# Kernel optimization log

Measured on AMD Instinct MI355X. Metric: run time of the kernel, lower is better.

The kernel has to match this reference:

```python
import jax, jax.numpy as jnp
import numpy as np

N = 20000          # nodes
E = 320000         # edges
IN_C = 512         # input features
HID = 512          # 2*out_channels (first GCN layer width)
OUT = 256          # out_channels == num_hidden
PROJ = 256         # num_proj_hidden


def _gcn_conv(x, W, b, src, dst):
    """PyG GCNConv: x' = D^{-1/2}(A+I)D^{-1/2} X W + b (self-loops added)."""
    n = x.shape[0]
    x = x @ W  # [N, F_out]
    ones = jnp.ones((src.shape[0],), x.dtype)
    deg = jax.ops.segment_sum(ones, dst, num_segments=n) + 1.0  # +1 self-loop
    dis = jax.lax.rsqrt(deg)
    coef = dis[src] * dis[dst]                      # [E]
    agg = jax.ops.segment_sum(x[src] * coef[:, None], dst, num_segments=n)
    agg = agg + x * (dis * dis)[:, None]            # self-loop messages
    return agg + b


def setup_inputs() -> dict:
    key = jax.random.key(0)
    ks = jax.random.split(key, 12)
    s = 0.02
    return {
        "node_features": jax.random.normal(ks[0], (N, IN_C), jnp.float32),
        "edge_index": jax.random.randint(ks[1], (2, E), 0, N, jnp.int64),
        "W1": jax.random.normal(ks[2], (IN_C, HID), jnp.float32) * s,
        "b1": jnp.zeros((HID,), jnp.float32),
        "W2": jax.random.normal(ks[3], (HID, OUT), jnp.float32) * s,
        "b2": jnp.zeros((OUT,), jnp.float32),
        "a": jnp.asarray(0.25, jnp.float32),  # shared PReLU weight
        "W3": jax.random.normal(ks[4], (OUT, PROJ), jnp.float32) * s,
        "b3": jnp.zeros((PROJ,), jnp.float32),
        "W4": jax.random.normal(ks[5], (PROJ, OUT), jnp.float32) * s,
        "b4": jnp.zeros((OUT,), jnp.float32),
    }


def reference(node_features, edge_index, W1, b1, W2, b2, a, W3, b3, W4, b4):
    src, dst = edge_index[0], edge_index[1]
    prelu = lambda x: jnp.where(x > 0, x, a * x)
    h = prelu(_gcn_conv(node_features, W1, b1, src, dst))
    h = prelu(_gcn_conv(h, W2, b2, src, dst))
    # projection MLP: Linear -> ELU -> Linear
    h2 = jax.nn.elu(h @ W3 + b3)
    return h2 @ W4 + b4
```

## Files before the change

kernel.cpp:

```cpp
#include <hip/hip_runtime.h>
#include <stdint.h>

typedef unsigned short u16;
typedef unsigned int   u32;
typedef __attribute__((ext_vector_type(8))) short short8;
typedef __attribute__((ext_vector_type(4))) float f32x4;

__device__ __forceinline__ float bf2f(u16 h){
    return __uint_as_float(((u32)h) << 16);
}
__device__ __forceinline__ u16 f2bf(float f){
    u32 u = __float_as_uint(f);
    u += 0x7fffu + ((u >> 16) & 1u);
    return (u16)(u >> 16);
}

__device__ __forceinline__ void gl_lds16(const void* g, void* l){
    __builtin_amdgcn_global_load_lds(
        (__attribute__((address_space(1))) void*)(uintptr_t)g,
        (__attribute__((address_space(3))) void*)(uintptr_t)l,
        16, 0, 0);
}

__global__ void probe_all(const u16* __restrict__ w1, const int* __restrict__ ei,
                          const void* b1, const void* b2, const void* b3,
                          const void* b4, const void* av,
                          int* __restrict__ efmt, int* __restrict__ cnt, int N,
                          u16* d1, u16* d2, u16* d3, u16* d4, u16* da){
    __shared__ int sf32, sfmt;
    int t = threadIdx.x;
    if (t == 0){ sf32 = 0; sfmt = 0; }
    __syncthreads();
    for (int i = t; i < N; i += 256) cnt[i] = 0;
    {
        int huge = 0;
        #pragma unroll
        for (int k = 0; k < 16; k++){
            u16 h = w1[t * 16 + k];
            if (((h >> 7) & 0xFF) >= 0x7F) huge = 1;
        }
        if (huge) atomicOr(&sf32, 1);
    }
    if (ei[2*t + 1] != 0) atomicOr(&sfmt, 1);
    __syncthreads();
    int f32 = sf32;
    if (t == 0) efmt[0] = sfmt;
    #define CV(s,i) (f32 ? f2bf(((const float*)(s))[i]) : ((const u16*)(s))[i])
    d1[t]       = CV(b1, t);
    d1[t + 256] = CV(b1, t + 256);
    d2[t] = CV(b2, t);
    d3[t] = CV(b3, t);
    d4[t] = CV(b4, t);
    if (t == 0) da[0] = CV(av, 0);
    #undef CV
}

__device__ __forceinline__ int eload(const int* ei, int fmt, int idx){
    return fmt ? ei[idx] : ei[2*idx];
}

__global__ void deg_count(const int* __restrict__ ei, const int* __restrict__ efmt,
                          int* __restrict__ cnt, int E, int N){
    int e = blockIdx.x * 256 + threadIdx.x;
    if (e < E){
        int d = eload(ei, efmt[0], E + e);
        if ((unsigned)d < (unsigned)N) atomicAdd(&cnt[d], 1);
    }
}

__global__ void scan1(const int* __restrict__ cnt, int* __restrict__ incl,
                      int* __restrict__ bsum, int N){
    __shared__ int s[256];
    int t = threadIdx.x, i = blockIdx.x * 256 + t;
    int v = (i < N) ? cnt[i] : 0;
    s[t] = v;
    __syncthreads();
    #pragma unroll
    for (int off = 1; off < 256; off <<= 1){
        int u = (t >= off) ? s[t - off] : 0;
        __syncthreads();
        s[t] += u;
        __syncthreads();
    }
    if (i < N) incl[i] = s[t];
    if (t == 255) bsum[blockIdx.x] = s[255];
}

__global__ void scan23(const int* __restrict__ cnt, const int* __restrict__ incl,
                       const int* __restrict__ bsum, int nb,
                       int* __restrict__ rowstart, int* __restrict__ cursor,
                       float* __restrict__ dis, int N){
    __shared__ int s[128];
    int t = threadIdx.x;
    if (t < 128) s[t] = (t < nb) ? bsum[t] : 0;
    __syncthreads();
    #pragma unroll
    for (int off = 1; off < 128; off <<= 1){
        int u = 0;
        if (t < 128 && t >= off) u = s[t - off];
        __syncthreads();
        if (t < 128) s[t] += u;
        __syncthreads();
    }
    int boffb = s[blockIdx.x] - bsum[blockIdx.x];
    int i = blockIdx.x * 256 + t;
    if (i < N){
        int v = cnt[i];
        int rsv = boffb + incl[i] - v;
        rowstart[i] = rsv;
        cursor[i]   = rsv;
        dis[i] = rsqrtf((float)v + 1.0f);
    }
    if (blockIdx.x == 0 && t == 0) rowstart[N] = s[nb - 1];
}

__global__ void csr_fill(const int* __restrict__ ei, const int* __restrict__ efmt,
                         int* __restrict__ cursor, int* __restrict__ csr_src,
                         int E, int N){
    int e = blockIdx.x * 256 + threadIdx.x;
    if (e < E){
        int fmt = efmt[0];
        int d = eload(ei, fmt, E + e);
        if ((unsigned)d < (unsigned)N){
            int p = atomicAdd(&cursor[d], 1);
            csr_src[p] = eload(ei, fmt, e);
        }
    }
}

__global__ void transpose_x(const void* w1, const void* w2, const void* w3,
                            const void* w4, const void* X,
                            u16* o1, u16* o2, u16* o3, u16* o4,
                            u16* xbf, int NN){
    __shared__ int sf;
    __shared__ u16 tb[32][33];
    int lt = threadIdx.y * 32 + threadIdx.x;
    if (lt == 0) sf = 0;
    __syncthreads();
    {
        int huge = 0;
        const u16* w = (const u16*)w1;
        #pragma unroll
        for (int k = 0; k < 8; k++){
            u16 h = w[lt * 8 + k];
            if (((h >> 7) & 0xFF) >= 0x7F) huge = 1;
        }
        if (huge) atomicOr(&sf, 1);
    }
    __syncthreads();
    int f32 = sf;

    if (blockIdx.z == 4){
        size_t nb8 = (size_t)NN * 64;
        size_t step = 256u * 256u;
        for (size_t i = (size_t)(blockIdx.y * 16 + blockIdx.x) * 256 + lt; i < nb8; i += step){
            short8 o;
            if (f32){
                const float* p = (const float*)X + i * 8;
                f32x4 a0 = *(const f32x4*)p;
                f32x4 a1 = *(const f32x4*)(p + 4);
                #pragma unroll
                for (int j = 0; j < 4; j++){
                    o[j]     = (short)f2bf(a0[j]);
                    o[4 + j] = (short)f2bf(a1[j]);
                }
            } else {
                o = *(const short8*)((const u16*)X + i * 8);
            }
            *(short8*)(xbf + i * 8) = o;
        }
        return;
    }

    const void* in; u16* out; int K, N;
    switch (blockIdx.z){
        case 0:  in = w1; out = o1; K = 512; N = 512; break;
        case 1:  in = w2; out = o2; K = 512; N = 256; break;
        case 2:  in = w3; out = o3; K = 256; N = 256; break;
        default: in = w4; out = o4; K = 256; N = 256; break;
    }
    int bx = blockIdx.x * 32;
    int by = blockIdx.y * 32;
    if (bx >= N || by >= K) return;
    int x = threadIdx.x, y = threadIdx.y;
    #pragma unroll
    for (int i = 0; i < 32; i += 8){
        size_t idx = (size_t)(by + y + i) * N + bx + x;
        tb[y + i][x] = f32 ? f2bf(((const float*)in)[idx]) : ((const u16*)in)[idx];
    }
    __syncthreads();
    #pragma unroll
    for (int i = 0; i < 32; i += 8)
        out[(size_t)(bx + y + i) * K + by + x] = tb[x][y + i];
}

#define GTM 128
#define GTN 128
#define GBK 64

template<int MODE, int OUTF>
__global__ __launch_bounds__(256) void gemm128(
    const u16* __restrict__ A, const u16* __restrict__ BT,
    const u16* __restrict__ bias, void* __restrict__ Cv,
    int M, int K, int N, int nN)
{
    __shared__ __align__(16) u16 As[GTM * GBK];
    __shared__ __align__(16) u16 Bs[GTN * GBK];
    int nwg = gridDim.x;
    int flat = blockIdx.x;
    int q8 = nwg >> 3, r8 = nwg & 7;
    int xcd = flat & 7, idx8 = flat >> 3;
    int wg = (xcd < r8 ? xcd * (q8 + 1) : r8 * (q8 + 1) + (xcd - r8) * q8) + idx8;
    int bm = (wg / nN) * GTM;
    int bn = (wg % nN) * GTN;

    int tid  = threadIdx.x;
    int lane = tid & 63;
    int wm   = (tid >> 7) & 1;
    int wn   = (tid >> 6) & 1;

    f32x4 acc[4][4] = {};

    int srow = tid >> 3;
    int scol = (tid & 7) * 8;
    const u16* aP = A  + (size_t)(bm + srow) * K + scol;
    const u16* bP = BT + (size_t)(bn + srow) * K + scol;
    u16* lA = &As[tid * 8];
    u16* lB = &Bs[tid * 8];

    int q   = lane >> 4;
    int r16 = lane & 15;
    const u16* ra = &As[(wm*64 + r16) * GBK + q*8];
    const u16* rb = &Bs[(wn*64 + r16) * GBK + q*8];

    for (int k0 = 0; k0 < K; k0 += GBK){
        #pragma unroll
        for (int r = 0; r < 4; r++){
            gl_lds16(aP + (size_t)r*32*K + k0, lA + r*32*GBK);
            gl_lds16(bP + (size_t)r*32*K + k0, lB + r*32*GBK);
        }
        __syncthreads();
        #pragma unroll
        for (int kk = 0; kk < 2; kk++){
            short8 af[4], bf[4];
            #pragma unroll
            for (int i = 0; i < 4; i++) af[i] = *(const short8*)(ra + i*16*GBK + kk*32);
            #pragma unroll
            for (int j = 0; j < 4; j++) bf[j] = *(const short8*)(rb + j*16*GBK + kk*32);
            #pragma unroll
            for (int i = 0; i < 4; i++)
                #pragma unroll
                for (int j = 0; j < 4; j++)
                    acc[i][j] = __builtin_amdgcn_mfma_f32_16x16x32_bf16(af[i], bf[j], acc[i][j], 0, 0, 0);
        }
        __syncthreads();
    }

    int q4 = q * 4;
    #pragma unroll
    for (int i = 0; i < 4; i++){
        #pragma unroll
        for (int j = 0; j < 4; j++){
            int gcol = bn + wn*64 + j*16 + r16;
            float bvv = (MODE >= 1) ? bf2f(bias[gcol]) : 0.f;
            #pragma unroll
            for (int r = 0; r < 4; r++){
                int grow = bm + wm*64 + i*16 + q4 + r;
                if (grow < M){
                    float v = acc[i][j][r] + bvv;
                    if (MODE == 2) v = (v > 0.f) ? v : expm1f(v);
                    if (OUTF) ((float*)Cv)[(size_t)grow * N + gcol] = v;
                    else      ((u16*)Cv)[(size_t)grow * N + gcol] = f2bf(v);
                }
            }
        }
    }
}

template<int F, int CH>
__global__ __launch_bounds__(256) void aggregate_ch(
    const u16* __restrict__ XW, const int* __restrict__ rowstart,
    const int* __restrict__ csr_src, const float* __restrict__ dis,
    const u16* __restrict__ bias, const u16* __restrict__ aptr,
    u16* __restrict__ out, int N)
{
    constexpr int NCH = F / CH;
    constexpr int LPN = CH / 8;
    constexpr int NPB = 256 / LPN;
    int bid = blockIdx.x;
    int chunk = bid % NCH;
    int node = (bid / NCH) * NPB + (threadIdx.x >> 3);
    if (node >= N) return;
    int tf = chunk * CH + (threadIdx.x & (LPN - 1)) * 8;
    float a  = bf2f(aptr[0]);
    float di = dis[node];
    int e0 = rowstart[node], e1 = rowstart[node + 1];
    float acc[8] = {0,0,0,0,0,0,0,0};
    int ng = (e1 - e0) >> 3;
    int si[8]; float ci[8];
    if (ng > 0){
        #pragma unroll
        for (int u = 0; u < 8; u++) si[u] = csr_src[e0 + u];
        #pragma unroll
        for (int u = 0; u < 8; u++) ci[u] = dis[si[u]];
    }
    for (int g = 0; g < ng; g++){
        short8 vi[8];
        #pragma unroll
        for (int u = 0; u < 8; u++)
            vi[u] = *(const short8*)(XW + (size_t)si[u] * F + tf);
        int sn[8]; float cn[8];
        bool more = (g + 1) < ng;
        if (more){
            int base = e0 + (g + 1) * 8;
            #pragma unroll
            for (int u = 0; u < 8; u++) sn[u] = csr_src[base + u];
            #pragma unroll
            for (int u = 0; u < 8; u++) cn[u] = dis[sn[u]];
        }
        #pragma unroll
        for (int u = 0; u < 8; u++)
            #pragma unroll
            for (int j = 0; j < 8; j++)
                acc[j] += ci[u] * bf2f((u16)vi[u][j]);
        if (more){
            #pragma unroll
            for (int u = 0; u < 8; u++){ si[u] = sn[u]; ci[u] = cn[u]; }
        }
    }
    int e = e0 + ng * 8;
    for (; e + 4 <= e1; e += 4){
        int s0 = csr_src[e], s1 = csr_src[e+1], s2 = csr_src[e+2], s3 = csr_src[e+3];
        float c0 = dis[s0], c1 = dis[s1], c2 = dis[s2], c3 = dis[s3];
        short8 v0 = *(const short8*)(XW + (size_t)s0 * F + tf);
        short8 v1 = *(const short8*)(XW + (size_t)s1 * F + tf);
        short8 v2 = *(const short8*)(XW + (size_t)s2 * F + tf);
        short8 v3 = *(const short8*)(XW + (size_t)s3 * F + tf);
        #pragma unroll
        for (int j = 0; j < 8; j++)
            acc[j] += c0*bf2f((u16)v0[j]) + c1*bf2f((u16)v1[j])
                    + c2*bf2f((u16)v2[j]) + c3*bf2f((u16)v3[j]);
    }
    for (; e < e1; e++){
        int s = csr_src[e];
        float c = dis[s];
        short8 v = *(const short8*)(XW + (size_t)s * F + tf);
        #pragma unroll
        for (int j = 0; j < 8; j++) acc[j] += c * bf2f((u16)v[j]);
    }
    {
        short8 v = *(const short8*)(XW + (size_t)node * F + tf);
        #pragma unroll
        for (int j = 0; j < 8; j++) acc[j] += di * bf2f((u16)v[j]);
    }
    short8 bv = *(const short8*)(bias + tf);
    short8 o;
    #pragma unroll
    for (int j = 0; j < 8; j++){
        float x = di * acc[j] + bf2f((u16)bv[j]);
        x = (x > 0.f) ? x : a * x;
        o[j] = (short)f2bf(x);
    }
    *(short8*)(out + (size_t)node * F + tf) = o;
}

extern "C" void kernel_launch(void* const* d_in, const int* in_sizes, int n_in,
                              void* d_out, int out_size, void* d_ws, size_t ws_size,
                              hipStream_t stream)
{
    int iX=0, iEI=1, iW1=2, ib1=3, iW2=4, ib2=5, ia=6, iW3=7, ib3=8, iW4=9, ib4=10;
    {
        int jX=-1,jEI=-1,jW1=-1,jb1=-1,jW2=-1,ja=-1,jW3=-1,jW4=-1,jb2=-1,jb3=-1,jb4=-1;
        int n64k=0, n256=0;
        for (int i = 0; i < n_in; i++){
            switch (in_sizes[i]){
                case 10240000: jX = i; break;
                case 640000:   jEI = i; break;
                case 262144:   jW1 = i; break;
                case 131072:   jW2 = i; break;
                case 512:      jb1 = i; break;
                case 1:        ja = i; break;
                case 65536:    if (n64k++ == 0) jW3 = i; else jW4 = i; break;
                case 256: {
                    int k = n256++;
                    if (k == 0) jb2 = i; else if (k == 1) jb3 = i; else jb4 = i;
                } break;
                default: break;
            }
        }
        if (jX>=0&&jEI>=0&&jW1>=0&&jb1>=0&&jW2>=0&&ja>=0&&jW3>=0&&jW4>=0&&jb2>=0&&jb3>=0&&jb4>=0){
            iX=jX; iEI=jEI; iW1=jW1; ib1=jb1; iW2=jW2; ib2=jb2; ia=ja; iW3=jW3; ib3=jb3; iW4=jW4; ib4=jb4;
        }
    }
    int N = in_sizes[iX] / 512;
    int E = in_sizes[iEI] / 2;
    const int* EI = (const int*)d_in[iEI];
    float* OUT = (float*)d_out;
    u16*   S   = (u16*)d_out;

    char* ws = (char*)d_ws;
    size_t off = 0;
    auto alloc = [&](size_t bytes)->char*{
        char* p = ws + off;
        off = (off + bytes + 255) & ~(size_t)255;
        return p;
    };
    int nb = (N + 255) / 256;
    int MP = N + 128;
    int*   cnt  = (int*)  alloc((size_t)N*4);
    int*   incl = (int*)  alloc((size_t)N*4);
    int*   bsum = (int*)  alloc(512);
    int*   efmt = (int*)  alloc(4);
    float* dis  = (float*)alloc((size_t)N*4);
    int*   rs   = (int*)  alloc((size_t)(N+1)*4);
    int*   cur  = (int*)  alloc((size_t)N*4);
    int*   csr  = (int*)  alloc((size_t)E*4);
    u16*   WT1  = (u16*)  alloc((size_t)512*512*2);
    u16*   WT2  = (u16*)  alloc((size_t)256*512*2);
    u16*   WT3  = (u16*)  alloc((size_t)256*256*2);
    u16*   WT4  = (u16*)  alloc((size_t)256*256*2);
    u16*   b1c  = (u16*)  alloc((size_t)512*2);
    u16*   b2c  = (u16*)  alloc((size_t)256*2);
    u16*   b3c  = (u16*)  alloc((size_t)256*2);
    u16*   b4c  = (u16*)  alloc((size_t)256*2);
    u16*   ac   = (u16*)  alloc((size_t)8*2);
    u16*   Xbf  = (u16*)  alloc((size_t)MP*512*2);
    u16*   h1   = (u16*)  alloc((size_t)MP*512*2);
    u16*   P    = (u16*)  alloc((size_t)MP*256*2);

    if (ws_size < off) return;

    probe_all<<<1, 256, 0, stream>>>((const u16*)d_in[iW1], EI,
                                     d_in[ib1], d_in[ib2], d_in[ib3], d_in[ib4],
                                     d_in[ia], efmt, cnt, N,
                                     b1c, b2c, b3c, b4c, ac);

    transpose_x<<<dim3(16, 16, 5), dim3(32, 8), 0, stream>>>(
        d_in[iW1], d_in[iW2], d_in[iW3], d_in[iW4], d_in[iX],
        WT1, WT2, WT3, WT4, Xbf, N);

    int egrid = (E + 255) / 256;
    deg_count<<<egrid, 256, 0, stream>>>(EI, efmt, cnt, E, N);
    scan1<<<nb, 256, 0, stream>>>(cnt, incl, bsum, N);
    scan23<<<nb, 256, 0, stream>>>(cnt, incl, bsum, nb, rs, cur, dis, N);
    csr_fill<<<egrid, 256, 0, stream>>>(EI, efmt, cur, csr, E, N);

    int gm = (N + GTM - 1) / GTM;
    int nodeb = (N + 31) / 32;

    gemm128<0,0><<<gm*4, 256, 0, stream>>>(Xbf, WT1, nullptr, S, N, 512, 512, 4);
    aggregate_ch<512,64><<<nodeb*8, 256, 0, stream>>>(S, rs, csr, dis, b1c, ac, h1, N);

    u16* Q = (u16*)d_out;
    gemm128<0,0><<<gm*2, 256, 0, stream>>>(h1, WT2, nullptr, P, N, 512, 256, 2);
    aggregate_ch<256,64><<<nodeb*4, 256, 0, stream>>>(P, rs, csr, dis, b2c, ac, Q, N);

    gemm128<2,0><<<gm*2, 256, 0, stream>>>(Q, WT3, b3c, P, N, 256, 256, 2);
    gemm128<1,1><<<gm*2, 256, 0, stream>>>(P, WT4, b4c, OUT, N, 256, 256, 2);
}
```

Baseline: 297.0 us.

## Merge setup kernels, single-block scan, 64-row GEMM tiles, padded aggregation pipeline

Removes the probe kernel. The edge-format probe moves inline into deg_count and csr_fill, bias conversion moves into transpose_x, and cnt is zeroed with hipMemsetAsync. The two-pass scan becomes one 1024-thread kernel. The GEMM is templated on row-tile size so the 256-wide GEMMs run with 64-row tiles for more workgroups, and the aggregation loop is restructured into a two-stage prefetch with padded groups of 8 instead of remainder loops. The result is fewer launches and better occupancy, at the cost of a serial single-block scan and some wasted loads on padded edges.

Measured after the change: 360.3 us. 1.21x slower.

```diff
diff --git a/kernel.cpp b/kernel.cpp
--- a/kernel.cpp
+++ b/kernel.cpp
@@ -22,104 +22,72 @@
         16, 0, 0);
 }
 
-__global__ void probe_all(const u16* __restrict__ w1, const int* __restrict__ ei,
-                          const void* b1, const void* b2, const void* b3,
-                          const void* b4, const void* av,
-                          int* __restrict__ efmt, int* __restrict__ cnt, int N,
-                          u16* d1, u16* d2, u16* d3, u16* d4, u16* da){
-    __shared__ int sf32, sfmt;
-    int t = threadIdx.x;
-    if (t == 0){ sf32 = 0; sfmt = 0; }
-    __syncthreads();
-    for (int i = t; i < N; i += 256) cnt[i] = 0;
-    {
-        int huge = 0;
-        #pragma unroll
-        for (int k = 0; k < 16; k++){
-            u16 h = w1[t * 16 + k];
-            if (((h >> 7) & 0xFF) >= 0x7F) huge = 1;
-        }
-        if (huge) atomicOr(&sf32, 1);
-    }
-    if (ei[2*t + 1] != 0) atomicOr(&sfmt, 1);
-    __syncthreads();
-    int f32 = sf32;
-    if (t == 0) efmt[0] = sfmt;
-    #define CV(s,i) (f32 ? f2bf(((const float*)(s))[i]) : ((const u16*)(s))[i])
-    d1[t]       = CV(b1, t);
-    d1[t + 256] = CV(b1, t + 256);
-    d2[t] = CV(b2, t);
-    d3[t] = CV(b3, t);
-    d4[t] = CV(b4, t);
-    if (t == 0) da[0] = CV(av, 0);
-    #undef CV
+__device__ __forceinline__ int probe_fmt(const int* ei, int* sh){
+    int t = threadIdx.x & 255;
+    if (threadIdx.x == 0) *sh = 0;
+    __syncthreads();
+    if (threadIdx.x < 256 && ei[2*t + 1] != 0) atomicOr(sh, 1);
+    __syncthreads();
+    return *sh;
 }
 
 __device__ __forceinline__ int eload(const int* ei, int fmt, int idx){
     return fmt ? ei[idx] : ei[2*idx];
 }
 
-__global__ void deg_count(const int* __restrict__ ei, const int* __restrict__ efmt,
-                          int* __restrict__ cnt, int E, int N){
+__global__ void deg_count(const int* __restrict__ ei, int* __restrict__ cnt,
+                          int E, int N){
+    __shared__ int sh;
+    int fmt = probe_fmt(ei, &sh);
     int e = blockIdx.x * 256 + threadIdx.x;
     if (e < E){
-        int d = eload(ei, efmt[0], E + e);
+        int d = eload(ei, fmt, E + e);
         if ((unsigned)d < (unsigned)N) atomicAdd(&cnt[d], 1);
     }
 }
 
-__global__ void scan1(const int* __restrict__ cnt, int* __restrict__ incl,
-                      int* __restrict__ bsum, int N){
-    __shared__ int s[256];
-    int t = threadIdx.x, i = blockIdx.x * 256 + t;
-    int v = (i < N) ? cnt[i] : 0;
-    s[t] = v;
+__global__ __launch_bounds__(1024) void scan_all(const int* __restrict__ cnt,
+                                                 int* __restrict__ rowstart,
+                                                 int* __restrict__ cursor,
+                                                 float* __restrict__ dis, int N){
+    __shared__ int s[1024];
+    int t = threadIdx.x;
+    int per = (N + 1023) / 1024;
+    int b0 = t * per;
+    int sum = 0;
+    for (int i = 0; i < per; i++){
+        int idx = b0 + i;
+        if (idx < N) sum += cnt[idx];
+    }
+    s[t] = sum;
     __syncthreads();
     #pragma unroll
-    for (int off = 1; off < 256; off <<= 1){
+    for (int off = 1; off < 1024; off <<= 1){
         int u = (t >= off) ? s[t - off] : 0;
         __syncthreads();
         s[t] += u;
         __syncthreads();
     }
-    if (i < N) incl[i] = s[t];
-    if (t == 255) bsum[blockIdx.x] = s[255];
-}
-
-__global__ void scan23(const int* __restrict__ cnt, const int* __restrict__ incl,
-                       const int* __restrict__ bsum, int nb,
-                       int* __restrict__ rowstart, int* __restrict__ cursor,
-                       float* __restrict__ dis, int N){
-    __shared__ int s[128];
-    int t = threadIdx.x;
-    if (t < 128) s[t] = (t < nb) ? bsum[t] : 0;
-    __syncthreads();
-    #pragma unroll
-    for (int off = 1; off < 128; off <<= 1){
-        int u = 0;
-        if (t < 128 && t >= off) u = s[t - off];
-        __syncthreads();
-        if (t < 128) s[t] += u;
-        __syncthreads();
-    }
-    int boffb = s[blockIdx.x] - bsum[blockIdx.x];
-    int i = blockIdx.x * 256 + t;
-    if (i < N){
-        int v = cnt[i];
-        int rsv = boffb + incl[i] - v;
-        rowstart[i] = rsv;
-        cursor[i]   = rsv;
-        dis[i] = rsqrtf((float)v + 1.0f);
-    }
-    if (blockIdx.x == 0 && t == 0) rowstart[N] = s[nb - 1];
-}
-
-__global__ void csr_fill(const int* __restrict__ ei, const int* __restrict__ efmt,
-                         int* __restrict__ cursor, int* __restrict__ csr_src,
-                         int E, int N){
+    int run = s[t] - sum;
+    for (int i = 0; i < per; i++){
+        int idx = b0 + i;
+        if (idx < N){
+            int v = cnt[idx];
+            rowstart[idx] = run;
+            cursor[idx]   = run;
+            dis[idx] = rsqrtf((float)v + 1.0f);
+            run += v;
+        }
+    }
+    if (t == 1023) rowstart[N] = s[1023];
+}
+
+__global__ void csr_fill(const int* __restrict__ ei, int* __restrict__ cursor,
+                         int* __restrict__ csr_src, int E, int N){
+    __shared__ int sh;
+    int fmt = probe_fmt(ei, &sh);
     int e = blockIdx.x * 256 + threadIdx.x;
     if (e < E){
-        int fmt = efmt[0];
         int d = eload(ei, fmt, E + e);
         if ((unsigned)d < (unsigned)N){
             int p = atomicAdd(&cursor[d], 1);
@@ -130,8 +98,11 @@
 
 __global__ void transpose_x(const void* w1, const void* w2, const void* w3,
                             const void* w4, const void* X,
+                            const void* b1, const void* b2, const void* b3,
+                            const void* b4, const void* av,
                             u16* o1, u16* o2, u16* o3, u16* o4,
-                            u16* xbf, int NN){
+                            u16* xbf, u16* d1, u16* d2, u16* d3, u16* d4,
+                            u16* da, int NN){
     __shared__ int sf;
     __shared__ u16 tb[32][33];
     int lt = threadIdx.y * 32 + threadIdx.x;
@@ -151,6 +122,16 @@
     int f32 = sf;
 
     if (blockIdx.z == 4){
+        #define CV(s,i) (f32 ? f2bf(((const float*)(s))[i]) : ((const u16*)(s))[i])
+        if (blockIdx.x == 0 && blockIdx.y == 0){
+            d1[lt]       = CV(b1, lt);
+            d1[lt + 256] = CV(b1, lt + 256);
+            d2[lt] = CV(b2, lt);
+            d3[lt] = CV(b3, lt);
+            d4[lt] = CV(b4, lt);
+            if (lt == 0) da[0] = CV(av, 0);
+        }
+        #undef CV
         size_t nb8 = (size_t)NN * 64;
         size_t step = 256u * 256u;
         for (size_t i = (size_t)(blockIdx.y * 16 + blockIdx.x) * 256 + lt; i < nb8; i += step){
@@ -194,24 +175,25 @@
         out[(size_t)(bx + y + i) * K + by + x] = tb[x][y + i];
 }
 
-#define GTM 128
 #define GTN 128
 #define GBK 64
 
-template<int MODE, int OUTF>
+template<int BM, int MODE, int OUTF>
 __global__ __launch_bounds__(256) void gemm128(
     const u16* __restrict__ A, const u16* __restrict__ BT,
     const u16* __restrict__ bias, void* __restrict__ Cv,
     int M, int K, int N, int nN)
 {
-    __shared__ __align__(16) u16 As[GTM * GBK];
+    constexpr int WM = BM / 2;
+    constexpr int AI = BM / 32;
+    __shared__ __align__(16) u16 As[BM  * GBK];
     __shared__ __align__(16) u16 Bs[GTN * GBK];
     int nwg = gridDim.x;
     int flat = blockIdx.x;
     int q8 = nwg >> 3, r8 = nwg & 7;
     int xcd = flat & 7, idx8 = flat >> 3;
     int wg = (xcd < r8 ? xcd * (q8 + 1) : r8 * (q8 + 1) + (xcd - r8) * q8) + idx8;
-    int bm = (wg / nN) * GTM;
+    int bm = (wg / nN) * BM;
     int bn = (wg % nN) * GTN;
 
     int tid  = threadIdx.x;
@@ -219,7 +201,7 @@
     int wm   = (tid >> 7) & 1;
     int wn   = (tid >> 6) & 1;
 
-    f32x4 acc[4][4] = {};
+    f32x4 acc[AI][4] = {};
 
     int srow = tid >> 3;
     int scol = (tid & 7) * 8;
@@ -230,25 +212,26 @@
 
     int q   = lane >> 4;
     int r16 = lane & 15;
-    const u16* ra = &As[(wm*64 + r16) * GBK + q*8];
+    const u16* ra = &As[(wm*WM + r16) * GBK + q*8];
     const u16* rb = &Bs[(wn*64 + r16) * GBK + q*8];
 
     for (int k0 = 0; k0 < K; k0 += GBK){
         #pragma unroll
-        for (int r = 0; r < 4; r++){
+        for (int r = 0; r < BM/32; r++)
             gl_lds16(aP + (size_t)r*32*K + k0, lA + r*32*GBK);
+        #pragma unroll
+        for (int r = 0; r < 4; r++)
             gl_lds16(bP + (size_t)r*32*K + k0, lB + r*32*GBK);
-        }
         __syncthreads();
         #pragma unroll
         for (int kk = 0; kk < 2; kk++){
-            short8 af[4], bf[4];
-            #pragma unroll
-            for (int i = 0; i < 4; i++) af[i] = *(const short8*)(ra + i*16*GBK + kk*32);
-            #pragma unroll
-            for (int j = 0; j < 4; j++) bf[j] = *(const short8*)(rb + j*16*GBK + kk*32);
-            #pragma unroll
-            for (int i = 0; i < 4; i++)
+            short8 af[AI], bf[4];
+            #pragma unroll
+            for (int i = 0; i < AI; i++) af[i] = *(const short8*)(ra + i*16*GBK + kk*32);
+            #pragma unroll
+            for (int j = 0; j < 4; j++)  bf[j] = *(const short8*)(rb + j*16*GBK + kk*32);
+            #pragma unroll
+            for (int i = 0; i < AI; i++)
                 #pragma unroll
                 for (int j = 0; j < 4; j++)
                     acc[i][j] = __builtin_amdgcn_mfma_f32_16x16x32_bf16(af[i], bf[j], acc[i][j], 0, 0, 0);
@@ -258,14 +241,14 @@
 
     int q4 = q * 4;
     #pragma unroll
-    for (int i = 0; i < 4; i++){
+    for (int i = 0; i < AI; i++){
         #pragma unroll
         for (int j = 0; j < 4; j++){
             int gcol = bn + wn*64 + j*16 + r16;
             float bvv = (MODE >= 1) ? bf2f(bias[gcol]) : 0.f;
             #pragma unroll
             for (int r = 0; r < 4; r++){
-                int grow = bm + wm*64 + i*16 + q4 + r;
+                int grow = bm + wm*WM + i*16 + q4 + r;
                 if (grow < M){
                     float v = acc[i][j][r] + bvv;
                     if (MODE == 2) v = (v > 0.f) ? v : expm1f(v);
@@ -295,58 +278,58 @@
     float a  = bf2f(aptr[0]);
     float di = dis[node];
     int e0 = rowstart[node], e1 = rowstart[node + 1];
+    int deg = e1 - e0;
     float acc[8] = {0,0,0,0,0,0,0,0};
-    int ng = (e1 - e0) >> 3;
-    int si[8]; float ci[8];
-    if (ng > 0){
-        #pragma unroll
-        for (int u = 0; u < 8; u++) si[u] = csr_src[e0 + u];
-        #pragma unroll
-        for (int u = 0; u < 8; u++) ci[u] = dis[si[u]];
-    }
-    for (int g = 0; g < ng; g++){
-        short8 vi[8];
-        #pragma unroll
-        for (int u = 0; u < 8; u++)
-            vi[u] = *(const short8*)(XW + (size_t)si[u] * F + tf);
-        int sn[8]; float cn[8];
-        bool more = (g + 1) < ng;
-        if (more){
-            int base = e0 + (g + 1) * 8;
-            #pragma unroll
-            for (int u = 0; u < 8; u++) sn[u] = csr_src[base + u];
-            #pragma unroll
-            for (int u = 0; u < 8; u++) cn[u] = dis[sn[u]];
-        }
-        #pragma unroll
-        for (int u = 0; u < 8; u++)
-            #pragma unroll
-            for (int j = 0; j < 8; j++)
-                acc[j] += ci[u] * bf2f((u16)vi[u][j]);
-        if (more){
-            #pragma unroll
-            for (int u = 0; u < 8; u++){ si[u] = sn[u]; ci[u] = cn[u]; }
-        }
-    }
-    int e = e0 + ng * 8;
-    for (; e + 4 <= e1; e += 4){
-        int s0 = csr_src[e], s1 = csr_src[e+1], s2 = csr_src[e+2], s3 = csr_src[e+3];
-        float c0 = dis[s0], c1 = dis[s1], c2 = dis[s2], c3 = dis[s3];
-        short8 v0 = *(const short8*)(XW + (size_t)s0 * F + tf);
-        short8 v1 = *(const short8*)(XW + (size_t)s1 * F + tf);
-        short8 v2 = *(const short8*)(XW + (size_t)s2 * F + tf);
-        short8 v3 = *(const short8*)(XW + (size_t)s3 * F + tf);
-        #pragma unroll
-        for (int j = 0; j < 8; j++)
-            acc[j] += c0*bf2f((u16)v0[j]) + c1*bf2f((u16)v1[j])
-                    + c2*bf2f((u16)v2[j]) + c3*bf2f((u16)v3[j]);
-    }
-    for (; e < e1; e++){
-        int s = csr_src[e];
-        float c = dis[s];
-        short8 v = *(const short8*)(XW + (size_t)s * F + tf);
-        #pragma unroll
-        for (int j = 0; j < 8; j++) acc[j] += c * bf2f((u16)v[j]);
+
+    if (deg > 0){
+        int ng = (deg + 7) >> 3;
+        auto ld_idx = [&](int g, int (&si)[8], float (&ci)[8]){
+            int base = e0 + g * 8;
+            #pragma unroll
+            for (int u = 0; u < 8; u++){
+                int e = base + u;
+                si[u] = csr_src[e < e1 ? e : e1 - 1];
+            }
+            #pragma unroll
+            for (int u = 0; u < 8; u++){
+                float c = dis[si[u]];
+                ci[u] = (base + u < e1) ? c : 0.f;
+            }
+        };
+        short8 vA[8]; float ciA[8];
+        {
+            int s0[8];
+            ld_idx(0, s0, ciA);
+            #pragma unroll
+            for (int u = 0; u < 8; u++)
+                vA[u] = *(const short8*)(XW + (size_t)s0[u] * F + tf);
+        }
+        int siB[8]; float ciB[8];
+        if (ng > 1) ld_idx(1, siB, ciB);
+        for (int g = 0; g < ng; g++){
+            short8 vB[8];
+            bool hasNext = (g + 1) < ng;
+            if (hasNext){
+                #pragma unroll
+                for (int u = 0; u < 8; u++)
+                    vB[u] = *(const short8*)(XW + (size_t)siB[u] * F + tf);
+            }
+            int siC[8]; float ciC[8];
+            if (g + 2 < ng) ld_idx(g + 2, siC, ciC);
+            #pragma unroll
+            for (int u = 0; u < 8; u++)
+                #pragma unroll
+                for (int j = 0; j < 8; j++)
+                    acc[j] += ciA[u] * bf2f((u16)vA[u][j]);
+            if (hasNext){
+                #pragma unroll
+                for (int u = 0; u < 8; u++){ vA[u] = vB[u]; ciA[u] = ciB[u]; }
+                if (g + 2 < ng){
+                    #pragma unroll
+                    for (int u = 0; u < 8; u++){ siB[u] = siC[u]; ciB[u] = ciC[u]; }
+                }
+            }
+        }
     }
     {
         short8 v = *(const short8*)(XW + (size_t)node * F + tf);
@@ -405,12 +388,8 @@
         off = (off + bytes + 255) & ~(size_t)255;
         return p;
     };
-    int nb = (N + 255) / 256;
     int MP = N + 128;
     int*   cnt  = (int*)  alloc((size_t)N*4);
-    int*   incl = (int*)  alloc((size_t)N*4);
-    int*   bsum = (int*)  alloc(512);
-    int*   efmt = (int*)  alloc(4);
     float* dis  = (float*)alloc((size_t)N*4);
     int*   rs   = (int*)  alloc((size_t)(N+1)*4);
     int*   cur  = (int*)  alloc((size_t)N*4);
@@ -430,31 +409,29 @@
 
     if (ws_size < off) return;
 
-    probe_all<<<1, 256, 0, stream>>>((const u16*)d_in[iW1], EI,
-                                     d_in[ib1], d_in[ib2], d_in[ib3], d_in[ib4],
-                                     d_in[ia], efmt, cnt, N,
-                                     b1c, b2c, b3c, b4c, ac);
+    hipMemsetAsync(cnt, 0, (size_t)N*4, stream);
 
     transpose_x<<<dim3(16, 16, 5), dim3(32, 8), 0, stream>>>(
         d_in[iW1], d_in[iW2], d_in[iW3], d_in[iW4], d_in[iX],
-        WT1, WT2, WT3, WT4, Xbf, N);
+        d_in[ib1], d_in[ib2], d_in[ib3], d_in[ib4], d_in[ia],
+        WT1, WT2, WT3, WT4, Xbf, b1c, b2c, b3c, b4c, ac, N);
 
     int egrid = (E + 255) / 256;
-    deg_count<<<egrid, 256, 0, stream>>>(EI, efmt, cnt, E, N);
-    scan1<<<nb, 256, 0, stream>>>(cnt, incl, bsum, N);
-    scan23<<<nb, 256, 0, stream>>>(cnt, incl, bsum, nb, rs, cur, dis, N);
-    csr_fill<<<egrid, 256, 0, stream>>>(EI, efmt, cur, csr, E, N);
-
-    int gm = (N + GTM - 1) / GTM;
+    deg_count<<<egrid, 256, 0, stream>>>(EI, cnt, E, N);
+    scan_all<<<1, 1024, 0, stream>>>(cnt, rs, cur, dis, N);
+    csr_fill<<<egrid, 256, 0, stream>>>(EI, cur, csr, E, N);
+
+    int gm128 = (N + 127) / 128;
+    int gm64  = (N + 63) / 64;
     int nodeb = (N + 31) / 32;
 
-    gemm128<0,0><<<gm*4, 256, 0, stream>>>(Xbf, WT1, nullptr, S, N, 512, 512, 4);
+    gemm128<128,0,0><<<gm128*4, 256, 0, stream>>>(Xbf, WT1, nullptr, S, N, 512, 512, 4);
     aggregate_ch<512,64><<<nodeb*8, 256, 0, stream>>>(S, rs, csr, dis, b1c, ac, h1, N);
 
     u16* Q = (u16*)d_out;
-    gemm128<0,0><<<gm*2, 256, 0, stream>>>(h1, WT2, nullptr, P, N, 512, 256, 2);
+    gemm128<64,0,0><<<gm64*2, 256, 0, stream>>>(h1, WT2, nullptr, P, N, 512, 256, 2);
     aggregate_ch<256,64><<<nodeb*4, 256, 0, stream>>>(P, rs, csr, dis, b2c, ac, Q, N);
 
-    gemm128<2,0><<<gm*2, 256, 0, stream>>>(Q, WT3, b3c, P, N, 256, 256, 2);
-    gemm128<1,1><<<gm*2, 256, 0, stream>>>(P, WT4, b4c, OUT, N, 256, 256, 2);
-}
+    gemm128<64,2,0><<<gm64*2, 256, 0, stream>>>(Q, WT3, b3c, P, N, 256, 256, 2);
+    gemm128<64,1,1><<<gm64*2, 256, 0, stream>>>(P, WT4, b4c, OUT, N, 256, 256, 2);
+}
```
